# Performance work log

Hardware: AMD Instinct MI355X
Metric: run time of the kernel (lower is better)

Reference implementation:

```python
import jax, jax.numpy as jnp
import numpy as np

NFEATS = 768; NHIDS = 768; H = 8; HD = NHIDS // H
NT = 32768; NC = 32768; NS = 32768; DEG = 8; E = NT * DEG
ALPHA = 0.2  # LeakyReLU negative slope


def setup_inputs() -> dict:
    key = jax.random.key(0)
    ks = jax.random.split(key, 16)
    f32 = jnp.float32
    dst = jnp.repeat(jnp.arange(NT, dtype=jnp.int32), DEG)  # uniform in-degree mailbox
    return {
        'h': jax.random.normal(ks[0], (NT, NFEATS), f32),
        'hb_c_src': jax.random.normal(ks[1], (NC, NHIDS), f32),
        'hb_s_src': jax.random.normal(ks[2], (NS, NHIDS), f32),
        'Wg': jax.random.normal(ks[3], (H, NFEATS, HD), f32) * 0.05,
        'bg': jnp.zeros((H, HD), f32),
        'ag': jax.random.normal(ks[4], (H, 2 * HD), f32) * 0.1,
        'agb': jnp.zeros((H,), f32),
        'Wx': jax.random.normal(ks[5], (H, NHIDS, HD), f32) * 0.05,
        'bx': jnp.zeros((H, HD), f32),
        'ax': jax.random.normal(ks[6], (H, 2 * HD), f32) * 0.1,
        'axb': jnp.zeros((H,), f32),
        'Wih': jax.random.normal(ks[7], (3 * NHIDS, NHIDS), f32) * 0.02,
        'Whh': jax.random.normal(ks[8], (3 * NHIDS, NHIDS), f32) * 0.02,
        'bih': jnp.zeros((3 * NHIDS,), f32),
        'bhh': jnp.zeros((3 * NHIDS,), f32),
        'intra_src': jax.random.randint(ks[9], (E,), 0, NT, jnp.int32),
        'intra_dst': dst,
        'c_src': jax.random.randint(ks[10], (E,), 0, NC, jnp.int32),
        'c_dst': dst,
        's_src': jax.random.randint(ks[11], (E,), 0, NS, jnp.int32),
        's_dst': dst,
    }


def _attend(Wh_s, Wh_d, src, dst, a, ab, n_dst):
    """Multi-head GAT edge attention + segment softmax + weighted aggregation.
    Wh_s: [Ns,H,D] src projections, Wh_d: [Nd,H,D] dst projections.
    a([Wh_src||Wh_dst]) decomposed as a_src.Wh_src + a_dst.Wh_dst + bias."""
    D = Wh_s.shape[-1]
    e = (jnp.einsum('nhd,hd->nh', Wh_s, a[:, :D])[src]
         + jnp.einsum('nhd,hd->nh', Wh_d, a[:, D:])[dst] + ab)  # [E,H]
    e = jax.nn.leaky_relu(e, ALPHA)
    m = jax.ops.segment_max(e, dst, num_segments=n_dst)
    ex = jnp.exp(e - m[dst])
    den = jax.ops.segment_sum(ex, dst, num_segments=n_dst)
    att = ex / den[dst]  # per-dst softmax over incoming edges (DGL mailbox softmax)
    out = jax.ops.segment_sum(Wh_s[src] * att[..., None], dst, num_segments=n_dst)
    return out.reshape(n_dst, H * D)  # concat heads


def _forward(h, hb_c_src, hb_s_src, Wg, bg, ag, agb, Wx, bx, ax, axb,
             Wih, Whh, bih, bhh, intra_src, intra_dst, c_src, c_dst, s_src, s_dst):
    n = h.shape[0]
    # intra-turn GAT (x = self.gat(g, t)); dropout is identity in eval mode
    Wh = jnp.einsum('nf,hfd->nhd', h, Wg) + bg
    x = _attend(Wh, Wh, intra_src, intra_dst, ag, agb, n)
    # cross-turn inversed GAT; dst nodes' 'hb' feature is the fresh gat output x;
    # counter_bw and support_bw share the same xgat weights.
    Wx_d = jnp.einsum('nf,hfd->nhd', x, Wx) + bx
    Wc_s = jnp.einsum('nf,hfd->nhd', hb_c_src, Wx) + bx
    h_c = _attend(Wc_s, Wx_d, c_src, c_dst, ax, axb, n)
    Ws_s = jnp.einsum('nf,hfd->nhd', hb_s_src, Wx) + bx
    h_s = _attend(Ws_s, Wx_d, s_src, s_dst, ax, axb, n)
    hid = 0.5 * h_c + 0.5 * h_s
    # GRUCell(x, hid)
    gi = x @ Wih.T + bih
    gh = hid @ Whh.T + bhh
    ir, iz, inn = jnp.split(gi, 3, axis=1)
    hr, hz, hn = jnp.split(gh, 3, axis=1)
    r = jax.nn.sigmoid(ir + hr)
    z = jax.nn.sigmoid(iz + hz)
    cand = jnp.tanh(inn + r * hn)
    return (1.0 - z) * cand + z * hid


def reference(h, hb_c_src, hb_s_src, Wg, bg, ag, agb, Wx, bx, ax, axb,
              Wih, Whh, bih, bhh, intra_src, intra_dst, c_src, c_dst, s_src, s_dst):
    return _forward(h, hb_c_src, hb_s_src, Wg, bg, ag, agb, Wx, bx, ax, axb,
                    Wih, Whh, bih, bhh, intra_src, intra_dst, c_src, c_dst, s_src, s_dst)
```

## Files before the change

kernel.cpp:

```cpp
#include <hip/hip_runtime.h>
#include <hip/hip_bf16.h>
#include <math.h>

#define NT 32768
#define HD 96
#define DEG 8
#define NE (NT * DEG)
#define LRELU_ALPHA 0.2f
#define CH 16384

typedef __attribute__((ext_vector_type(8))) short bf16x8;
typedef __attribute__((ext_vector_type(8))) unsigned short u16x8;
typedef __attribute__((ext_vector_type(4))) unsigned short u16x4;
typedef __attribute__((ext_vector_type(4))) float f32x4;

__device__ __forceinline__ unsigned short f2bf(float x) {
    union { float f; unsigned u; } v; v.f = x;
    unsigned r = v.u + 0x7FFFu + ((v.u >> 16) & 1u);
    return (unsigned short)(r >> 16);
}
__device__ __forceinline__ float bf2f(unsigned short u) {
    union { unsigned u; float f; } v; v.u = ((unsigned)u) << 16; return v.f;
}

__device__ __forceinline__ void gload_lds16(const void* g, void* l) {
    __builtin_amdgcn_global_load_lds(
        (const __attribute__((address_space(1))) void*)g,
        (__attribute__((address_space(3))) void*)l, 16, 0, 0);
}


__global__ void packWT(const float* __restrict__ W, unsigned short* __restrict__ T) {
    int idx = blockIdx.x * 256 + threadIdx.x;
    if (idx >= 768 * 768) return;
    int c = idx / 768, f = idx % 768;
    T[idx] = f2bf(W[(size_t)(c / HD) * 768 * HD + (size_t)f * HD + (c % HD)]);
}

__global__ void cvt_bf8(const float* __restrict__ X, unsigned short* __restrict__ Y, int n8) {
    int i = blockIdx.x * 256 + threadIdx.x;
    if (i >= n8) return;
    float4 a = ((const float4*)X)[2 * i];
    float4 b = ((const float4*)X)[2 * i + 1];
    u16x8 p;
    p[0] = f2bf(a.x); p[1] = f2bf(a.y); p[2] = f2bf(a.z); p[3] = f2bf(a.w);
    p[4] = f2bf(b.x); p[5] = f2bf(b.y); p[6] = f2bf(b.z); p[7] = f2bf(b.w);
    ((u16x8*)Y)[i] = p;
}

__global__ void packWV(const float* __restrict__ Wx, const float* __restrict__ ax,
                       const float* __restrict__ bx,
                       float* __restrict__ wv, float* __restrict__ cd) {
    int idx = blockIdx.x * 256 + threadIdx.x;
    if (idx < 8 * 768) {
        int h = idx / 768, f = idx % 768;
        const float* wp = Wx + (size_t)h * 768 * HD + (size_t)f * HD;
        const float* ap = ax + h * 2 * HD + HD;
        float s = 0.f;
        for (int d = 0; d < HD; d++) s += wp[d] * ap[d];
        wv[idx] = s;
    }
    if (idx < 8) {
        const float* bp = bx + idx * HD;
        const float* ap = ax + idx * 2 * HD + HD;
        float s = 0.f;
        for (int d = 0; d < HD; d++) s += bp[d] * ap[d];
        cd[idx] = s;
    }
}

__global__ __launch_bounds__(256, 4) void mgemm_bb(
    const unsigned short* __restrict__ A, const unsigned short* __restrict__ BT,
    const float* __restrict__ bias, unsigned short* __restrict__ C,
    int M, int N, int K) {
    __shared__ unsigned short Alds[2][128 * 32];
    __shared__ unsigned short Blds[2][128 * 32];
    const int tid = threadIdx.x;
    const int w = tid >> 6, l = tid & 63;
    const int wr = w >> 1, wc = w & 1;
    const int lrow = l & 15, lk = l >> 4;

    const int nx = gridDim.x;
    const int nwg = nx * gridDim.y;
    int lin = blockIdx.y * nx + blockIdx.x;
    if ((nwg & 7) == 0) lin = (lin & 7) * (nwg >> 3) + (lin >> 3);
    const int bm = lin / nx, bn = lin % nx;

    const unsigned short* asrc[2];
    const unsigned short* bsrc[2];
    #pragma unroll
    for (int q = 0; q < 2; q++) {
        int idx = q * 256 + tid;
        int r = idx >> 2, s = idx & 3;
        int kw = s ^ ((r >> 1) & 3);
        asrc[q] = A  + (size_t)(bm * 128 + r) * K + kw * 8;
        bsrc[q] = BT + (size_t)(bn * 128 + r) * K + kw * 8;
    }
    const int ldst = (w * 64) * 8;

    gload_lds16(asrc[0], &Alds[0][ldst]);
    gload_lds16(asrc[1], &Alds[0][2048 + ldst]);
    gload_lds16(bsrc[0], &Blds[0][ldst]);
    gload_lds16(bsrc[1], &Blds[0][2048 + ldst]);

    f32x4 acc[4][4] = {};
    const int nt = K >> 5;

    for (int t = 0; t < nt; ++t) {
        const int cur = t & 1;
        __syncthreads();
        if (t + 1 < nt) {
            const int k1 = (t + 1) << 5;
            gload_lds16(asrc[0] + k1, &Alds[cur ^ 1][ldst]);
            gload_lds16(asrc[1] + k1, &Alds[cur ^ 1][2048 + ldst]);
            gload_lds16(bsrc[0] + k1, &Blds[cur ^ 1][ldst]);
            gload_lds16(bsrc[1] + k1, &Blds[cur ^ 1][2048 + ldst]);
        }
        bf16x8 af[4], bfv[4];
        #pragma unroll
        for (int i = 0; i < 4; i++) {
            int r = wr * 64 + i * 16 + lrow;
            int s = lk ^ ((r >> 1) & 3);
            af[i] = *(const bf16x8*)(&Alds[cur][r * 32 + s * 8]);
        }
        #pragma unroll
        for (int j = 0; j < 4; j++) {
            int r = wc * 64 + j * 16 + lrow;
            int s = lk ^ ((r >> 1) & 3);
            bfv[j] = *(const bf16x8*)(&Blds[cur][r * 32 + s * 8]);
        }
        #pragma unroll
        for (int i = 0; i < 4; i++)
            #pragma unroll
            for (int j = 0; j < 4; j++)
                acc[i][j] = __builtin_amdgcn_mfma_f32_16x16x32_bf16(af[i], bfv[j], acc[i][j], 0, 0, 0);
    }

    const size_t crow0 = (size_t)bm * 128 + wr * 64;
    const int ccol0 = bn * 128 + wc * 64;
    #pragma unroll
    for (int j = 0; j < 4; j++) {
        int col = ccol0 + j * 16 + lrow;
        float bv = bias[col];
        #pragma unroll
        for (int i = 0; i < 4; i++) {
            size_t row = crow0 + i * 16 + lk * 4;
            #pragma unroll
            for (int e = 0; e < 4; e++)
                C[(row + e) * N + col] = f2bf(acc[i][j][e] + bv);
        }
    }
}

__global__ __launch_bounds__(256) void escore2(
    const unsigned short* __restrict__ X, const float* __restrict__ a,
    float* __restrict__ s0out, float* __restrict__ s1out) {
    __shared__ float av0[768], av1[768];
    for (int t = threadIdx.x; t < 768; t += 256) {
        int hh = t / HD, d = t % HD;
        av0[t] = a[hh * 2 * HD + d];
        av1[t] = a[hh * 2 * HD + HD + d];
    }
    __syncthreads();
    int idx = blockIdx.x * 256 + threadIdx.x;
    int row = idx >> 3, hh = idx & 7;
    const unsigned short* xp = X + (size_t)row * 768 + hh * HD;
    const float* a0 = av0 + hh * HD;
    const float* a1 = av1 + hh * HD;
    float s0 = 0.f, s1 = 0.f;
    #pragma unroll
    for (int q = 0; q < 12; q++) {
        u16x8 v = *(const u16x8*)(xp + q * 8);
        #pragma unroll
        for (int e = 0; e < 8; e++) {
            float x = bf2f(v[e]);
            s0 += x * a0[q * 8 + e];
            s1 += x * a1[q * 8 + e];
        }
    }
    s0out[idx] = s0;
    s1out[idx] = s1;
}

__global__ __launch_bounds__(256) void escore(
    const unsigned short* __restrict__ X, const float* __restrict__ a,
    int half, float* __restrict__ sc) {
    __shared__ float av[768];
    for (int t = threadIdx.x; t < 768; t += 256) {
        int hh = t / HD, d = t % HD;
        av[t] = a[hh * 2 * HD + half * HD + d];
    }
    __syncthreads();
    int idx = blockIdx.x * 256 + threadIdx.x;
    int row = idx >> 3, hh = idx & 7;
    const unsigned short* xp = X + (size_t)row * 768 + hh * HD;
    const float* ap = av + hh * HD;
    float s = 0.f;
    #pragma unroll
    for (int q = 0; q < 12; q++) {
        u16x8 v = *(const u16x8*)(xp + q * 8);
        #pragma unroll
        for (int e = 0; e < 8; e++) s += bf2f(v[e]) * ap[q * 8 + e];
    }
    sc[idx] = s;
}

__global__ __launch_bounds__(256) void escore_fold(
    const unsigned short* __restrict__ X, const float* __restrict__ wv,
    const float* __restrict__ cd, float* __restrict__ ed) {
    __shared__ float wvs[8][8][97];
    __shared__ float cds[8];
    for (int i = threadIdx.x; i < 8 * 8 * 96; i += 256) {
        int j = i / (8 * 96); int r = i % (8 * 96); int h = r / 96; int t = r % 96;
        wvs[j][h][t] = wv[h * 768 + j * 96 + t];
    }
    if (threadIdx.x < 8) cds[threadIdx.x] = cd[threadIdx.x];
    __syncthreads();
    int idx = blockIdx.x * 256 + threadIdx.x;
    int n = idx >> 3, j = idx & 7;
    const unsigned short* xp = X + (size_t)n * 768 + j * 96;
    float p[8] = {};
    #pragma unroll
    for (int q = 0; q < 12; q++) {
        u16x8 v = *(const u16x8*)(xp + q * 8);
        #pragma unroll
        for (int e = 0; e < 8; e++) {
            float x = bf2f(v[e]);
            #pragma unroll
            for (int h = 0; h < 8; h++) p[h] += x * wvs[j][h][q * 8 + e];
        }
    }
    #pragma unroll
    for (int o = 1; o < 8; o <<= 1)
        #pragma unroll
        for (int h = 0; h < 8; h++) p[h] += __shfl_xor(p[h], o, 64);
    ed[(size_t)n * 8 + j] = p[j] + cds[j];
}

__global__ __launch_bounds__(256) void attend_agg(
    const unsigned short* __restrict__ Whs, const float* __restrict__ es,
    const float* __restrict__ ed, const float* __restrict__ ab,
    const int* __restrict__ src, const int* __restrict__ dst,
    unsigned short* __restrict__ out) {
    const int wv = threadIdx.x >> 6, l = threadIdx.x & 63;
    const int seg = blockIdx.x * 4 + wv;
    const int hh = l >> 3, j = l & 7;
    int sj = src[seg * 8 + j];
    int dnode = dst[seg * 8];
    float e = es[(size_t)sj * 8 + hh] + ed[(size_t)dnode * 8 + hh] + ab[hh];
    e = e > 0.f ? e : LRELU_ALPHA * e;
    float m = e;
    #pragma unroll
    for (int o = 1; o < 8; o <<= 1) m = fmaxf(m, __shfl_xor(m, o, 64));
    float ex = expf(e - m);
    float s = ex;
    #pragma unroll
    for (int o = 1; o < 8; o <<= 1) s += __shfl_xor(s, o, 64);
    float att = ex / s;

    #pragma unroll
    for (int u = 0; u < 3; u++) {
        int c = 4 * l + 256 * u;
        int h = c / HD;
        float acc0 = 0.f, acc1 = 0.f, acc2 = 0.f, acc3 = 0.f;
        #pragma unroll
        for (int j2 = 0; j2 < 8; j2++) {
            float a = __shfl(att, h * 8 + j2, 64);
            int sid = __shfl(sj, j2, 64);
            u16x4 v = *(const u16x4*)(Whs + (size_t)sid * 768 + c);
            acc0 += a * bf2f(v[0]); acc1 += a * bf2f(v[1]);
            acc2 += a * bf2f(v[2]); acc3 += a * bf2f(v[3]);
        }
        u16x4 r;
        r[0] = f2bf(acc0); r[1] = f2bf(acc1); r[2] = f2bf(acc2); r[3] = f2bf(acc3);
        *(u16x4*)(out + (size_t)dnode * 768 + c) = r;
    }
}

__global__ __launch_bounds__(256) void attend2(
    const unsigned short* __restrict__ Wc, const unsigned short* __restrict__ Ws,
    const float* __restrict__ esC, const float* __restrict__ esS,
    const float* __restrict__ ed, const float* __restrict__ ab,
    const int* __restrict__ csrc, const int* __restrict__ ssrc,
    const int* __restrict__ dst, unsigned short* __restrict__ outH) {
    const int wv = threadIdx.x >> 6, l = threadIdx.x & 63;
    const int seg = blockIdx.x * 4 + wv;
    const int hh = l >> 3, j = l & 7;
    int cj = csrc[seg * 8 + j];
    int sj = ssrc[seg * 8 + j];
    int dnode = dst[seg * 8];
    float edv = ed[(size_t)dnode * 8 + hh] + ab[hh];

    float eC = esC[(size_t)cj * 8 + hh] + edv;
    eC = eC > 0.f ? eC : LRELU_ALPHA * eC;
    float mC = eC;
    #pragma unroll
    for (int o = 1; o < 8; o <<= 1) mC = fmaxf(mC, __shfl_xor(mC, o, 64));
    float exC = expf(eC - mC);
    float sC = exC;
    #pragma unroll
    for (int o = 1; o < 8; o <<= 1) sC += __shfl_xor(sC, o, 64);
    float attC = exC / sC;

    float eS = esS[(size_t)sj * 8 + hh] + edv;
    eS = eS > 0.f ? eS : LRELU_ALPHA * eS;
    float mS = eS;
    #pragma unroll
    for (int o = 1; o < 8; o <<= 1) mS = fmaxf(mS, __shfl_xor(mS, o, 64));
    float exS = expf(eS - mS);
    float sS = exS;
    #pragma unroll
    for (int o = 1; o < 8; o <<= 1) sS += __shfl_xor(sS, o, 64);
    float attS = exS / sS;

    #pragma unroll
    for (int u = 0; u < 3; u++) {
        int c = 4 * l + 256 * u;
        int h = c / HD;
        float acc0 = 0.f, acc1 = 0.f, acc2 = 0.f, acc3 = 0.f;
        #pragma unroll
        for (int j2 = 0; j2 < 8; j2++) {
            float a = __shfl(attC, h * 8 + j2, 64);
            int sid = __shfl(cj, j2, 64);
            u16x4 v = *(const u16x4*)(Wc + (size_t)sid * 768 + c);
            acc0 += a * bf2f(v[0]); acc1 += a * bf2f(v[1]);
            acc2 += a * bf2f(v[2]); acc3 += a * bf2f(v[3]);
        }
        #pragma unroll
        for (int j2 = 0; j2 < 8; j2++) {
            float a = __shfl(attS, h * 8 + j2, 64);
            int sid = __shfl(sj, j2, 64);
            u16x4 v = *(const u16x4*)(Ws + (size_t)sid * 768 + c);
            acc0 += a * bf2f(v[0]); acc1 += a * bf2f(v[1]);
            acc2 += a * bf2f(v[2]); acc3 += a * bf2f(v[3]);
        }
        u16x4 r;
        r[0] = f2bf(0.5f * acc0); r[1] = f2bf(0.5f * acc1);
        r[2] = f2bf(0.5f * acc2); r[3] = f2bf(0.5f * acc3);
        *(u16x4*)(outH + (size_t)dnode * 768 + c) = r;
    }
}

__global__ __launch_bounds__(256) void gru_elem(
    const unsigned short* __restrict__ gi, const unsigned short* __restrict__ gh,
    const unsigned short* __restrict__ hid, float* __restrict__ out) {
    int idx = blockIdx.x * 256 + threadIdx.x;
    int nrow = idx / 96, c8 = (idx % 96) * 8;
    const unsigned short* gip = gi + (size_t)nrow * 2304 + c8;
    const unsigned short* ghp = gh + (size_t)nrow * 2304 + c8;
    u16x8 vir = *(const u16x8*)(gip);
    u16x8 viz = *(const u16x8*)(gip + 768);
    u16x8 vin = *(const u16x8*)(gip + 1536);
    u16x8 vhr = *(const u16x8*)(ghp);
    u16x8 vhz = *(const u16x8*)(ghp + 768);
    u16x8 vhn = *(const u16x8*)(ghp + 1536);
    u16x8 vh  = *(const u16x8*)(hid + (size_t)nrow * 768 + c8);
    float res[8];
    #pragma unroll
    for (int e = 0; e < 8; e++) {
        float r = 1.f / (1.f + expf(-(bf2f(vir[e]) + bf2f(vhr[e]))));
        float z = 1.f / (1.f + expf(-(bf2f(viz[e]) + bf2f(vhz[e]))));
        float cand = tanhf(bf2f(vin[e]) + r * bf2f(vhn[e]));
        res[e] = (1.f - z) * cand + z * bf2f(vh[e]);
    }
    float* op = out + (size_t)nrow * 768 + c8;
    *(float4*)(op)     = make_float4(res[0], res[1], res[2], res[3]);
    *(float4*)(op + 4) = make_float4(res[4], res[5], res[6], res[7]);
}

extern "C" void kernel_launch(void* const* d_in, const int* in_sizes, int n_in,
                              void* d_out, int out_size, void* d_ws, size_t ws_size,
                              hipStream_t stream) {
    const float* h    = (const float*)d_in[0];
    const float* hbc  = (const float*)d_in[1];
    const float* hbs  = (const float*)d_in[2];
    const float* Wg   = (const float*)d_in[3];
    const float* bg   = (const float*)d_in[4];
    const float* ag   = (const float*)d_in[5];
    const float* agb  = (const float*)d_in[6];
    const float* Wx   = (const float*)d_in[7];
    const float* bx   = (const float*)d_in[8];
    const float* ax   = (const float*)d_in[9];
    const float* axb  = (const float*)d_in[10];
    const float* Wih  = (const float*)d_in[11];
    const float* Whh  = (const float*)d_in[12];
    const float* bih  = (const float*)d_in[13];
    const float* bhh  = (const float*)d_in[14];
    const int* i_src  = (const int*)d_in[15];
    const int* i_dst  = (const int*)d_in[16];
    const int* c_src  = (const int*)d_in[17];
    const int* c_dst  = (const int*)d_in[18];
    const int* s_src  = (const int*)d_in[19];
    const int* s_dst  = (const int*)d_in[20];
    float* out = (float*)d_out;

    const size_t SZ = (size_t)NT * 768;
    unsigned short* Xb   = (unsigned short*)d_ws;
    unsigned short* Hdb  = Xb + SZ;
    unsigned short* GIb  = Hdb + SZ;
    unsigned short* GHb  = GIb + (size_t)CH * 2304;
    unsigned short* ABc  = GIb;
    unsigned short* ABs  = GIb + SZ;
    unsigned short* W2gT = GHb + (size_t)CH * 2304;
    unsigned short* W2xT = W2gT + 768 * 768;
    unsigned short* WihB = W2xT + 768 * 768;
    unsigned short* WhhB = WihB + 2304 * 768;
    float* EScat = (float*)(WhhB + 2304 * 768);
    float* ED    = EScat + 2 * NE;
    float* ESI   = ED + NE;
    float* EDI   = ESI + NE;
    float* WV    = EDI + NE;
    float* CD    = WV + 8 * 768;
    unsigned short* Pcat = (unsigned short*)d_out;

    dim3 blk(256);
    packWT<<<(768 * 768 + 255) / 256, blk, 0, stream>>>(Wg, W2gT);
    packWT<<<(768 * 768 + 255) / 256, blk, 0, stream>>>(Wx, W2xT);
    cvt_bf8<<<(2304 * 768 / 8 + 255) / 256, blk, 0, stream>>>(Wih, WihB, 2304 * 768 / 8);
    cvt_bf8<<<(2304 * 768 / 8 + 255) / 256, blk, 0, stream>>>(Whh, WhhB, 2304 * 768 / 8);
    packWV<<<(8 * 768 + 255) / 256, blk, 0, stream>>>(Wx, ax, bx, WV, CD);

    dim3 g768(6, NT / 128);
    dim3 gcat(6, 2 * NT / 128);
    const int n8 = (int)(SZ / 8);
    const int cvtg = (n8 + 255) / 256;

    cvt_bf8<<<cvtg, blk, 0, stream>>>(h, ABc, n8);
    mgemm_bb<<<g768, blk, 0, stream>>>(ABc, W2gT, bg, Pcat, NT, 768, 768);
    escore2<<<NE / 256, blk, 0, stream>>>(Pcat, ag, ESI, EDI);
    attend_agg<<<NT / 4, blk, 0, stream>>>(Pcat, ESI, EDI, agb, i_src, i_dst, Xb);
    escore_fold<<<NE / 256, blk, 0, stream>>>(Xb, WV, CD, ED);
    cvt_bf8<<<cvtg, blk, 0, stream>>>(hbc, ABc, n8);
    cvt_bf8<<<cvtg, blk, 0, stream>>>(hbs, ABs, n8);
    mgemm_bb<<<gcat, blk, 0, stream>>>(ABc, W2xT, bx, Pcat, 2 * NT, 768, 768);
    escore<<<2 * NE / 256, blk, 0, stream>>>(Pcat, ax, 0, EScat);
    attend2<<<NT / 4, blk, 0, stream>>>(Pcat, Pcat + SZ, EScat, EScat + NE, ED, axb,
                                        c_src, s_src, c_dst, Hdb);
    dim3 gch(2304 / 128, CH / 128);
    for (int c0 = 0; c0 < NT; c0 += CH) {
        mgemm_bb<<<gch, blk, 0, stream>>>(Xb  + (size_t)c0 * 768, WihB, bih, GIb, CH, 2304, 768);
        mgemm_bb<<<gch, blk, 0, stream>>>(Hdb + (size_t)c0 * 768, WhhB, bhh, GHb, CH, 2304, 768);
        gru_elem<<<(CH * 96) / 256, blk, 0, stream>>>(GIb, GHb, Hdb + (size_t)c0 * 768, out + (size_t)c0 * 768);
    }
}
```

Before: 927.1 us.

## Use 256x256x64 GEMM tiles and batch paired GEMMs into single launches

Replaces the 128x128x32 bf16 MFMA GEMM with a 512-thread kernel using 256x256 output tiles and a 64-wide K step, with setprio around the MFMA block. The kernel takes two A/B/bias/C sets and picks one per block by row-tile index. This lets the three input projections run in one launch and each GRU chunk's two gate GEMMs run in one launch. Larger tiles raise arithmetic intensity and cut launches, but the LDS footprint of 128 KB per block limits occupancy to one block per CU. The grid has fewer blocks, which may hurt tail balance.

```diff
diff --git a/kernel.cpp b/kernel.cpp
--- a/kernel.cpp
+++ b/kernel.cpp
@@ -69,81 +69,98 @@
     }
 }
 
-__global__ __launch_bounds__(256, 4) void mgemm_bb(
-    const unsigned short* __restrict__ A, const unsigned short* __restrict__ BT,
-    const float* __restrict__ bias, unsigned short* __restrict__ C,
-    int M, int N, int K) {
-    __shared__ unsigned short Alds[2][128 * 32];
-    __shared__ unsigned short Blds[2][128 * 32];
+__global__ __launch_bounds__(512, 2) void mgemm3(
+    const unsigned short* __restrict__ A1, const unsigned short* __restrict__ A2,
+    const unsigned short* __restrict__ BT1, const unsigned short* __restrict__ BT2,
+    const float* __restrict__ bias1, const float* __restrict__ bias2,
+    unsigned short* __restrict__ C1, unsigned short* __restrict__ C2,
+    int mt1, int N, int K) {
+    __shared__ unsigned short Alds[2][256 * 64];
+    __shared__ unsigned short Blds[2][256 * 64];
     const int tid = threadIdx.x;
     const int w = tid >> 6, l = tid & 63;
-    const int wr = w >> 1, wc = w & 1;
+    const int wr = w >> 2, wc = w & 3;
     const int lrow = l & 15, lk = l >> 4;
 
     const int nx = gridDim.x;
     const int nwg = nx * gridDim.y;
     int lin = blockIdx.y * nx + blockIdx.x;
     if ((nwg & 7) == 0) lin = (lin & 7) * (nwg >> 3) + (lin >> 3);
-    const int bm = lin / nx, bn = lin % nx;
-
-    const unsigned short* asrc[2];
-    const unsigned short* bsrc[2];
-    #pragma unroll
-    for (int q = 0; q < 2; q++) {
-        int idx = q * 256 + tid;
-        int r = idx >> 2, s = idx & 3;
-        int kw = s ^ ((r >> 1) & 3);
-        asrc[q] = A  + (size_t)(bm * 128 + r) * K + kw * 8;
-        bsrc[q] = BT + (size_t)(bn * 128 + r) * K + kw * 8;
-    }
-    const int ldst = (w * 64) * 8;
-
-    gload_lds16(asrc[0], &Alds[0][ldst]);
-    gload_lds16(asrc[1], &Alds[0][2048 + ldst]);
-    gload_lds16(bsrc[0], &Blds[0][ldst]);
-    gload_lds16(bsrc[1], &Blds[0][2048 + ldst]);
-
-    f32x4 acc[4][4] = {};
-    const int nt = K >> 5;
+    int bm = lin / nx;
+    const int bn = lin % nx;
+
+    const bool p1 = bm < mt1;
+    const unsigned short* A  = p1 ? A1 : A2;
+    const unsigned short* BT = p1 ? BT1 : BT2;
+    const float* bias        = p1 ? bias1 : bias2;
+    unsigned short* C        = p1 ? C1 : C2;
+    if (!p1) bm -= mt1;
+
+    const unsigned short* asrc[4];
+    const unsigned short* bsrc[4];
+    #pragma unroll
+    for (int q = 0; q < 4; q++) {
+        int idx = q * 512 + tid;
+        int r = idx >> 3, s = idx & 7;
+        int kw = s ^ ((r >> 1) & 7);
+        asrc[q] = A  + (size_t)(bm * 256 + r) * K + kw * 8;
+        bsrc[q] = BT + (size_t)(bn * 256 + r) * K + kw * 8;
+    }
+    const int ldst = w * 512;
+
+    f32x4 acc[8][4] = {};
+    const int nt = K >> 6;
+
+    #pragma unroll
+    for (int q = 0; q < 4; q++) {
+        gload_lds16(asrc[q], &Alds[0][q * 4096 + ldst]);
+        gload_lds16(bsrc[q], &Blds[0][q * 4096 + ldst]);
+    }
 
     for (int t = 0; t < nt; ++t) {
         const int cur = t & 1;
         __syncthreads();
         if (t + 1 < nt) {
-            const int k1 = (t + 1) << 5;
-            gload_lds16(asrc[0] + k1, &Alds[cur ^ 1][ldst]);
-            gload_lds16(asrc[1] + k1, &Alds[cur ^ 1][2048 + ldst]);
-            gload_lds16(bsrc[0] + k1, &Blds[cur ^ 1][ldst]);
-            gload_lds16(bsrc[1] + k1, &Blds[cur ^ 1][2048 + ldst]);
-        }
-        bf16x8 af[4], bfv[4];
-        #pragma unroll
-        for (int i = 0; i < 4; i++) {
-            int r = wr * 64 + i * 16 + lrow;
-            int s = lk ^ ((r >> 1) & 3);
-            af[i] = *(const bf16x8*)(&Alds[cur][r * 32 + s * 8]);
-        }
-        #pragma unroll
-        for (int j = 0; j < 4; j++) {
-            int r = wc * 64 + j * 16 + lrow;
-            int s = lk ^ ((r >> 1) & 3);
-            bfv[j] = *(const bf16x8*)(&Blds[cur][r * 32 + s * 8]);
-        }
-        #pragma unroll
-        for (int i = 0; i < 4; i++)
-            #pragma unroll
-            for (int j = 0; j < 4; j++)
-                acc[i][j] = __builtin_amdgcn_mfma_f32_16x16x32_bf16(af[i], bfv[j], acc[i][j], 0, 0, 0);
-    }
-
-    const size_t crow0 = (size_t)bm * 128 + wr * 64;
-    const int ccol0 = bn * 128 + wc * 64;
+            const int k1 = (t + 1) << 6;
+            #pragma unroll
+            for (int q = 0; q < 4; q++) {
+                gload_lds16(asrc[q] + k1, &Alds[cur ^ 1][q * 4096 + ldst]);
+                gload_lds16(bsrc[q] + k1, &Blds[cur ^ 1][q * 4096 + ldst]);
+            }
+        }
+        #pragma unroll
+        for (int ks = 0; ks < 2; ks++) {
+            bf16x8 bfv[4], af[8];
+            #pragma unroll
+            for (int j = 0; j < 4; j++) {
+                int r = wc * 64 + j * 16 + lrow;
+                int s = (ks * 4 + lk) ^ ((r >> 1) & 7);
+                bfv[j] = *(const bf16x8*)(&Blds[cur][r * 64 + s * 8]);
+            }
+            #pragma unroll
+            for (int i = 0; i < 8; i++) {
+                int r = wr * 128 + i * 16 + lrow;
+                int s = (ks * 4 + lk) ^ ((r >> 1) & 7);
+                af[i] = *(const bf16x8*)(&Alds[cur][r * 64 + s * 8]);
+            }
+            __builtin_amdgcn_s_setprio(1);
+            #pragma unroll
+            for (int i = 0; i < 8; i++)
+                #pragma unroll
+                for (int j = 0; j < 4; j++)
+                    acc[i][j] = __builtin_amdgcn_mfma_f32_16x16x32_bf16(af[i], bfv[j], acc[i][j], 0, 0, 0);
+            __builtin_amdgcn_s_setprio(0);
+        }
+    }
+
+    const size_t crow0 = (size_t)bm * 256 + wr * 128;
+    const int ccol0 = bn * 256 + wc * 64;
     #pragma unroll
     for (int j = 0; j < 4; j++) {
         int col = ccol0 + j * 16 + lrow;
         float bv = bias[col];
         #pragma unroll
-        for (int i = 0; i < 4; i++) {
+        for (int i = 0; i < 8; i++) {
             size_t row = crow0 + i * 16 + lk * 4;
             #pragma unroll
             for (int e = 0; e < 4; e++)
@@ -399,8 +416,9 @@
     unsigned short* Hdb  = Xb + SZ;
     unsigned short* GIb  = Hdb + SZ;
     unsigned short* GHb  = GIb + (size_t)CH * 2304;
-    unsigned short* ABc  = GIb;
-    unsigned short* ABs  = GIb + SZ;
+    unsigned short* ABh  = GIb;
+    unsigned short* ABc  = GIb + SZ;
+    unsigned short* ABs  = GIb + 2 * SZ;
     unsigned short* W2gT = GHb + (size_t)CH * 2304;
     unsigned short* W2xT = W2gT + 768 * 768;
     unsigned short* WihB = W2xT + 768 * 768;
@@ -414,32 +432,34 @@
     unsigned short* Pcat = (unsigned short*)d_out;
 
     dim3 blk(256);
+    dim3 blk512(512);
     packWT<<<(768 * 768 + 255) / 256, blk, 0, stream>>>(Wg, W2gT);
     packWT<<<(768 * 768 + 255) / 256, blk, 0, stream>>>(Wx, W2xT);
     cvt_bf8<<<(2304 * 768 / 8 + 255) / 256, blk, 0, stream>>>(Wih, WihB, 2304 * 768 / 8);
     cvt_bf8<<<(2304 * 768 / 8 + 255) / 256, blk, 0, stream>>>(Whh, WhhB, 2304 * 768 / 8);
     packWV<<<(8 * 768 + 255) / 256, blk, 0, stream>>>(Wx, ax, bx, WV, CD);
 
-    dim3 g768(6, NT / 128);
-    dim3 gcat(6, 2 * NT / 128);
     const int n8 = (int)(SZ / 8);
     const int cvtg = (n8 + 255) / 256;
 
-    cvt_bf8<<<cvtg, blk, 0, stream>>>(h, ABc, n8);
-    mgemm_bb<<<g768, blk, 0, stream>>>(ABc, W2gT, bg, Pcat, NT, 768, 768);
-    escore2<<<NE / 256, blk, 0, stream>>>(Pcat, ag, ESI, EDI);
-    attend_agg<<<NT / 4, blk, 0, stream>>>(Pcat, ESI, EDI, agb, i_src, i_dst, Xb);
-    escore_fold<<<NE / 256, blk, 0, stream>>>(Xb, WV, CD, ED);
+    cvt_bf8<<<cvtg, blk, 0, stream>>>(h,   ABh, n8);
     cvt_bf8<<<cvtg, blk, 0, stream>>>(hbc, ABc, n8);
     cvt_bf8<<<cvtg, blk, 0, stream>>>(hbs, ABs, n8);
-    mgemm_bb<<<gcat, blk, 0, stream>>>(ABc, W2xT, bx, Pcat, 2 * NT, 768, 768);
+
+    dim3 gproj(3, 384);
+    mgemm3<<<gproj, blk512, 0, stream>>>(ABh, ABc, W2gT, W2xT, bg, bx,
+                                         Hdb, Pcat, 128, 768, 768);
+    escore2<<<NE / 256, blk, 0, stream>>>(Hdb, ag, ESI, EDI);
+    attend_agg<<<NT / 4, blk, 0, stream>>>(Hdb, ESI, EDI, agb, i_src, i_dst, Xb);
+    escore_fold<<<NE / 256, blk, 0, stream>>>(Xb, WV, CD, ED);
     escore<<<2 * NE / 256, blk, 0, stream>>>(Pcat, ax, 0, EScat);
     attend2<<<NT / 4, blk, 0, stream>>>(Pcat, Pcat + SZ, EScat, EScat + NE, ED, axb,
                                         c_src, s_src, c_dst, Hdb);
-    dim3 gch(2304 / 128, CH / 128);
+    dim3 ggru(9, 128);
     for (int c0 = 0; c0 < NT; c0 += CH) {
-        mgemm_bb<<<gch, blk, 0, stream>>>(Xb  + (size_t)c0 * 768, WihB, bih, GIb, CH, 2304, 768);
-        mgemm_bb<<<gch, blk, 0, stream>>>(Hdb + (size_t)c0 * 768, WhhB, bhh, GHb, CH, 2304, 768);
+        mgemm3<<<ggru, blk512, 0, stream>>>(Xb + (size_t)c0 * 768, Hdb + (size_t)c0 * 768,
+                                            WihB, WhhB, bih, bhh, GIb, GHb,
+                                            64, 2304, 768);
         gru_elem<<<(CH * 96) / 256, blk, 0, stream>>>(GIb, GHb, Hdb + (size_t)c0 * 768, out + (size_t)c0 * 768);
     }
 }
```

Result: slower. 990.9 us (+6.9%).
